# Kernel tuning notes

Measured on AMD Instinct MI355X. Metric: run time of the kernel, lower is better.

Reference implementation:

```python
import jax, jax.numpy as jnp
import numpy as np

LN_EPS = 1e-5

def _layernorm(x, gamma, beta):
    mu = jnp.mean(x, axis=-1, keepdims=True)
    var = jnp.mean(jnp.square(x - mu), axis=-1, keepdims=True)
    return (x - mu) * jax.lax.rsqrt(var + LN_EPS) * gamma + beta


def setup_inputs() -> dict:
    key = jax.random.key(0)
    k1, k2 = jax.random.split(key)
    B, T, E = 8, 4096, 1024
    half = E // 2
    kernel = 15
    x = jax.random.normal(k1, (B, T, E), dtype=jnp.float32)
    weight = jax.random.normal(k2, (half, kernel), dtype=jnp.float32) * 0.02
    gamma = jnp.ones((half,), dtype=jnp.float32)
    beta = jnp.zeros((half,), dtype=jnp.float32)
    return {"x": x, "weight": weight, "gamma": gamma, "beta": beta}


def reference(x, weight, gamma, beta):
    # x: [B, T, E]; split into residual and gate halves along channels
    res, gate = jnp.split(x, 2, axis=-1)          # each [B, T, C], C = E//2
    gate = _layernorm(gate, gamma, beta)
    n = gate.shape[1]
    gate = jnp.transpose(gate, (0, 2, 1))         # [B, C, T]
    gate_f = jnp.fft.rfft(gate, n=n, axis=-1)     # [B, C, n//2+1] complex
    w_f = jnp.fft.rfft(weight, n=n, axis=-1)      # [C, n//2+1] complex
    # (gr*wr + gi*wi) + i(gi*wr - gr*wi) == gate_f * conj(w_f)
    prod = gate_f * jnp.conj(w_f)
    gate = jnp.fft.irfft(prod, n=n, axis=-1)      # [B, C, T]
    gate = jnp.transpose(gate, (0, 2, 1))         # [B, T, C]
    # act is Identity
    return gate * res
```

## Files before the change

### kernel.cpp

```cpp
#include <hip/hip_runtime.h>

#define T_DIM 4096
#define C_DIM 512
#define E_DIM 1024
#define KW 15
#define LN_EPS 1e-5f

#define TB 32
#define RT (TB + KW - 1)
#define NW 8

__global__ __launch_bounds__(512) void fgu_prep_kernel(
    const float* __restrict__ w,
    const float* __restrict__ gamma,
    const float* __restrict__ beta,
    float* __restrict__ wpad)
{
    const int c = threadIdx.x;
    const float gm = gamma[c];
    const float bt = beta[c];
    float s = 0.0f;
    float* o = wpad + c * 16;
    #pragma unroll
    for (int j = 0; j < KW; ++j) {
        const float wj = w[c * KW + j];
        s += wj;
        o[j] = gm * wj;
    }
    o[KW] = bt * s;
}

__global__ __launch_bounds__(512, 4) void fgu_fused_kernel(
    const float* __restrict__ x,
    const float* __restrict__ wpad,
    float* __restrict__ out)
{
    __shared__ float2 srn[RT];

    const int tid  = threadIdx.x;
    const int lane = tid & 63;
    const int wv   = tid >> 6;
    const int b    = blockIdx.x >> 7;
    const int t0   = (blockIdx.x & 127) * TB;

    const float* xb = x + (size_t)b * T_DIM * E_DIM;

    for (int k = wv; k < RT; k += NW) {
        const int tt = (t0 + k) & (T_DIM - 1);
        const float* gp = xb + (size_t)tt * E_DIM + C_DIM;
        const float4 a  = *(const float4*)(gp + lane * 4);
        const float4 b4 = *(const float4*)(gp + 256 + lane * 4);

        float s  = a.x + a.y + a.z + a.w + b4.x + b4.y + b4.z + b4.w;
        float ss = a.x*a.x + a.y*a.y + a.z*a.z + a.w*a.w
                 + b4.x*b4.x + b4.y*b4.y + b4.z*b4.z + b4.w*b4.w;
        #pragma unroll
        for (int off = 32; off; off >>= 1) {
            s  += __shfl_xor(s, off);
            ss += __shfl_xor(ss, off);
        }
        if (lane == 0) {
            const float mu  = s * (1.0f / (float)C_DIM);
            const float var = ss * (1.0f / (float)C_DIM) - mu * mu;
            const float rs  = rsqrtf(var + LN_EPS);
            srn[k] = make_float2(rs, -mu * rs);
        }
    }
    __syncthreads();

    const int c = tid;
    const float* gc = xb + C_DIM + c;

    float z[RT];
    #pragma unroll
    for (int k = 0; k < RT; ++k) {
        const int tt = (t0 + k) & (T_DIM - 1);
        const float2 p = srn[k];
        z[k] = fmaf(gc[(size_t)tt * E_DIM], p.x, p.y);
    }

    float wr[16];
    {
        const float4* wp = (const float4*)(wpad + c * 16);
        const float4 w0 = wp[0], w1 = wp[1], w2 = wp[2], w3 = wp[3];
        wr[0]=w0.x;  wr[1]=w0.y;  wr[2]=w0.z;  wr[3]=w0.w;
        wr[4]=w1.x;  wr[5]=w1.y;  wr[6]=w1.z;  wr[7]=w1.w;
        wr[8]=w2.x;  wr[9]=w2.y;  wr[10]=w2.z; wr[11]=w2.w;
        wr[12]=w3.x; wr[13]=w3.y; wr[14]=w3.z; wr[15]=w3.w;
    }

    const float* rb = xb + (size_t)t0 * E_DIM + c;
    float*       ob = out + ((size_t)b * T_DIM + t0) * C_DIM + c;
    #pragma unroll
    for (int i = 0; i < TB; ++i) {
        float acc = wr[KW];
        #pragma unroll
        for (int j = 0; j < KW; ++j)
            acc = fmaf(z[i + j], wr[j], acc);
        ob[(size_t)i * C_DIM] = rb[(size_t)i * E_DIM] * acc;
    }
}

extern "C" void kernel_launch(void* const* d_in, const int* in_sizes, int n_in,
                              void* d_out, int out_size, void* d_ws, size_t ws_size,
                              hipStream_t stream) {
    const float* x      = (const float*)d_in[0];
    const float* weight = (const float*)d_in[1];
    const float* gamma  = (const float*)d_in[2];
    const float* beta   = (const float*)d_in[3];
    float* out  = (float*)d_out;
    float* wpad = (float*)d_ws;

    fgu_prep_kernel<<<1, 512, 0, stream>>>(weight, gamma, beta, wpad);

    const int nblocks = 8 * (T_DIM / TB);
    fgu_fused_kernel<<<nblocks, 512, 0, stream>>>(x, wpad, out);
}
```

Before: 236.5 us.

## Split layernorm stats into separate kernel and vectorize correlation over two channels

Moves per-row layernorm mean/rstd computation into its own kernel that writes a stats array to workspace, removing the redundant halo recomputation and block-level sync from the correlation kernel. The correlation kernel now uses 256 threads, each handling two adjacent channels with float2 loads and stores, and the time tile shrinks from 32 to 16. The price is an extra launch, a second read of the gate half of x, and a larger halo-to-tile ratio with the smaller tile.

```diff
diff --git a/kernel.cpp b/kernel.cpp
--- a/kernel.cpp
+++ b/kernel.cpp
@@ -6,9 +6,8 @@
 #define KW 15
 #define LN_EPS 1e-5f
 
-#define TB 32
+#define TB 16
 #define RT (TB + KW - 1)
-#define NW 8
 
 __global__ __launch_bounds__(512) void fgu_prep_kernel(
     const float* __restrict__ w,
@@ -30,74 +29,83 @@
     o[KW] = bt * s;
 }
 
-__global__ __launch_bounds__(512, 4) void fgu_fused_kernel(
+__global__ __launch_bounds__(256) void fgu_stats_kernel(
     const float* __restrict__ x,
+    float2* __restrict__ stats)
+{
+    const int row  = (int)((blockIdx.x * blockDim.x + threadIdx.x) >> 6);
+    const int lane = threadIdx.x & 63;
+
+    const float* gp = x + (size_t)row * E_DIM + C_DIM;
+    const float4 a  = *(const float4*)(gp + lane * 4);
+    const float4 b4 = *(const float4*)(gp + 256 + lane * 4);
+
+    float s  = a.x + a.y + a.z + a.w + b4.x + b4.y + b4.z + b4.w;
+    float ss = a.x*a.x + a.y*a.y + a.z*a.z + a.w*a.w
+             + b4.x*b4.x + b4.y*b4.y + b4.z*b4.z + b4.w*b4.w;
+    #pragma unroll
+    for (int off = 32; off; off >>= 1) {
+        s  += __shfl_xor(s, off);
+        ss += __shfl_xor(ss, off);
+    }
+    if (lane == 0) {
+        const float mu  = s * (1.0f / (float)C_DIM);
+        const float var = ss * (1.0f / (float)C_DIM) - mu * mu;
+        const float rs  = rsqrtf(var + LN_EPS);
+        stats[row] = make_float2(rs, -mu * rs);
+    }
+}
+
+__global__ __launch_bounds__(256) void fgu_corr_kernel(
+    const float* __restrict__ x,
+    const float2* __restrict__ stats,
     const float* __restrict__ wpad,
     float* __restrict__ out)
 {
-    __shared__ float2 srn[RT];
-
-    const int tid  = threadIdx.x;
-    const int lane = tid & 63;
-    const int wv   = tid >> 6;
-    const int b    = blockIdx.x >> 7;
-    const int t0   = (blockIdx.x & 127) * TB;
+    const int tid = threadIdx.x;
+    const int b   = blockIdx.x >> 8;
+    const int t0  = (blockIdx.x & 255) * TB;
+    const int c   = tid * 2;
 
     const float* xb = x + (size_t)b * T_DIM * E_DIM;
+    const float2* sb = stats + ((size_t)b << 12);
 
-    for (int k = wv; k < RT; k += NW) {
-        const int tt = (t0 + k) & (T_DIM - 1);
-        const float* gp = xb + (size_t)tt * E_DIM + C_DIM;
-        const float4 a  = *(const float4*)(gp + lane * 4);
-        const float4 b4 = *(const float4*)(gp + 256 + lane * 4);
-
-        float s  = a.x + a.y + a.z + a.w + b4.x + b4.y + b4.z + b4.w;
-        float ss = a.x*a.x + a.y*a.y + a.z*a.z + a.w*a.w
-                 + b4.x*b4.x + b4.y*b4.y + b4.z*b4.z + b4.w*b4.w;
-        #pragma unroll
-        for (int off = 32; off; off >>= 1) {
-            s  += __shfl_xor(s, off);
-            ss += __shfl_xor(ss, off);
-        }
-        if (lane == 0) {
-            const float mu  = s * (1.0f / (float)C_DIM);
-            const float var = ss * (1.0f / (float)C_DIM) - mu * mu;
-            const float rs  = rsqrtf(var + LN_EPS);
-            srn[k] = make_float2(rs, -mu * rs);
-        }
-    }
-    __syncthreads();
-
-    const int c = tid;
+    float2 z[RT];
     const float* gc = xb + C_DIM + c;
-
-    float z[RT];
     #pragma unroll
     for (int k = 0; k < RT; ++k) {
         const int tt = (t0 + k) & (T_DIM - 1);
-        const float2 p = srn[k];
-        z[k] = fmaf(gc[(size_t)tt * E_DIM], p.x, p.y);
+        const float2 g = *(const float2*)(gc + (size_t)tt * E_DIM);
+        const float2 p = sb[tt];
+        z[k].x = fmaf(g.x, p.x, p.y);
+        z[k].y = fmaf(g.y, p.x, p.y);
     }
 
-    float wr[16];
+    float wr0[16], wr1[16];
     {
         const float4* wp = (const float4*)(wpad + c * 16);
-        const float4 w0 = wp[0], w1 = wp[1], w2 = wp[2], w3 = wp[3];
-        wr[0]=w0.x;  wr[1]=w0.y;  wr[2]=w0.z;  wr[3]=w0.w;
-        wr[4]=w1.x;  wr[5]=w1.y;  wr[6]=w1.z;  wr[7]=w1.w;
-        wr[8]=w2.x;  wr[9]=w2.y;  wr[10]=w2.z; wr[11]=w2.w;
-        wr[12]=w3.x; wr[13]=w3.y; wr[14]=w3.z; wr[15]=w3.w;
+        #pragma unroll
+        for (int q = 0; q < 4; ++q) {
+            const float4 v0 = wp[q];
+            const float4 v1 = wp[q + 4];
+            wr0[q*4+0] = v0.x; wr0[q*4+1] = v0.y; wr0[q*4+2] = v0.z; wr0[q*4+3] = v0.w;
+            wr1[q*4+0] = v1.x; wr1[q*4+1] = v1.y; wr1[q*4+2] = v1.z; wr1[q*4+3] = v1.w;
+        }
     }
 
     const float* rb = xb + (size_t)t0 * E_DIM + c;
     float*       ob = out + ((size_t)b * T_DIM + t0) * C_DIM + c;
     #pragma unroll
     for (int i = 0; i < TB; ++i) {
-        float acc = wr[KW];
+        float a0 = wr0[KW];
+        float a1 = wr1[KW];
         #pragma unroll
-        for (int j = 0; j < KW; ++j)
-            acc = fmaf(z[i + j], wr[j], acc);
-        ob[(size_t)i * C_DIM] = rb[(size_t)i * E_DIM] * acc;
+        for (int j = 0; j < KW; ++j) {
+            a0 = fmaf(z[i + j].x, wr0[j], a0);
+            a1 = fmaf(z[i + j].y, wr1[j], a1);
+        }
+        const float2 r = *(const float2*)(rb + (size_t)i * E_DIM);
+        *(float2*)(ob + (size_t)i * C_DIM) = make_float2(r.x * a0, r.y * a1);
     }
 }
 
@@ -108,11 +116,16 @@
     const float* weight = (const float*)d_in[1];
     const float* gamma  = (const float*)d_in[2];
     const float* beta   = (const float*)d_in[3];
-    float* out  = (float*)d_out;
-    float* wpad = (float*)d_ws;
+    float* out = (float*)d_out;
+
+    float*  wpad  = (float*)d_ws;
+    float2* stats = (float2*)((char*)d_ws + 512 * 16 * sizeof(float));
 
     fgu_prep_kernel<<<1, 512, 0, stream>>>(weight, gamma, beta, wpad);
 
+    const int nrows = 8 * T_DIM;
+    fgu_stats_kernel<<<nrows / 4, 256, 0, stream>>>(x, stats);
+
     const int nblocks = 8 * (T_DIM / TB);
-    fgu_fused_kernel<<<nblocks, 512, 0, stream>>>(x, wpad, out);
+    fgu_corr_kernel<<<nblocks, 256, 0, stream>>>(x, stats, wpad, out);
 }
```

New measurement: 242.0 us. 2.3% more time.
